# Performance work log

Measured on AMD Instinct MI355X. Metric: run time of the kernel, lower is better.

## Reference

```python
import jax, jax.numpy as jnp
import numpy as np

NEG_SLOPE = 0.01  # torch leaky_relu default
EPS = 1e-12      # torch F.normalize default


def _edge_mlp(edge_attr, w1, b1, w2, b2, d_h):
    # Sequential(Linear, ReLU, Linear) -> per-edge weight matrices [E, d_h, d_h]
    h = jax.nn.relu(edge_attr @ w1 + b1)
    return (h @ w2 + b2).reshape(-1, d_h, d_h)


def _nnconv(h, src, dst, w_edge, root, bias, n_nodes):
    # message_j->i = x_j @ Theta(e_ji); aggregate (add) at dst; add root transform + bias
    msg = jnp.einsum('ei,eio->eo', h[src], w_edge)  # [E, d_h]
    agg = jax.ops.segment_sum(msg, dst, num_segments=n_nodes)
    return agg + h @ root + bias


def setup_inputs() -> dict:
    key = jax.random.key(0)
    ks = jax.random.split(key, 20)
    N, E, G = 20000, 200000, 128
    d_node, d_edge, d_h, d_out = 64, 16, 32, 32

    x = jax.random.normal(ks[0], (N, d_node), dtype=jnp.float32)
    edge_index = jax.random.randint(ks[1], (2, E), 0, N, dtype=jnp.int32)
    edge_attr = jax.random.normal(ks[2], (E, d_edge), dtype=jnp.float32)
    batch = jnp.sort(jax.random.randint(ks[3], (N,), 0, G, dtype=jnp.int32))

    def lin(k, fan_in, fan_out):
        kw, kb = jax.random.split(k)
        s = 1.0 / np.sqrt(fan_in)
        w = jax.random.uniform(kw, (fan_in, fan_out), jnp.float32, -s, s)
        b = jax.random.uniform(kb, (fan_out,), jnp.float32, -s, s)
        return w, b

    nfc_w, nfc_b = lin(ks[4], d_node, d_h)
    efc1_w1, efc1_b1 = lin(ks[5], d_edge, d_h)
    efc1_w2, efc1_b2 = lin(ks[6], d_h, d_h * d_h)
    root1 = jax.random.uniform(ks[7], (d_h, d_h), jnp.float32, -1/np.sqrt(d_h), 1/np.sqrt(d_h))
    bias1 = jnp.zeros((d_h,), jnp.float32)
    efc2_w1, efc2_b1 = lin(ks[8], d_edge, d_h)
    efc2_w2, efc2_b2 = lin(ks[9], d_h, d_h * d_h)
    root2 = jax.random.uniform(ks[10], (d_h, d_h), jnp.float32, -1/np.sqrt(d_h), 1/np.sqrt(d_h))
    bias2 = jnp.zeros((d_h,), jnp.float32)
    fc_w, fc_b = lin(ks[11], d_h, d_out)

    return dict(x=x, edge_index=edge_index, edge_attr=edge_attr, batch=batch,
                num_graphs=G,
                nfc_w=nfc_w, nfc_b=nfc_b,
                efc1_w1=efc1_w1, efc1_b1=efc1_b1, efc1_w2=efc1_w2, efc1_b2=efc1_b2,
                root1=root1, bias1=bias1,
                efc2_w1=efc2_w1, efc2_b1=efc2_b1, efc2_w2=efc2_w2, efc2_b2=efc2_b2,
                root2=root2, bias2=bias2,
                fc_w=fc_w, fc_b=fc_b)


def reference(x, edge_index, edge_attr, batch, num_graphs,
              nfc_w, nfc_b,
              efc1_w1, efc1_b1, efc1_w2, efc1_b2, root1, bias1,
              efc2_w1, efc2_b1, efc2_w2, efc2_b2, root2, bias2,
              fc_w, fc_b):
    n_nodes = x.shape[0]
    d_h = nfc_w.shape[1]
    src, dst = edge_index[0], edge_index[1]

    lrelu = lambda v: jax.nn.leaky_relu(v, NEG_SLOPE)
    # dropout(p=0.1) is identity at inference
    h = lrelu(x @ nfc_w + nfc_b)

    w_e1 = _edge_mlp(edge_attr, efc1_w1, efc1_b1, efc1_w2, efc1_b2, d_h)
    h = lrelu(_nnconv(h, src, dst, w_e1, root1, bias1, n_nodes))

    w_e2 = _edge_mlp(edge_attr, efc2_w1, efc2_b1, efc2_w2, efc2_b2, d_h)
    atom_embs = lrelu(_nnconv(h, src, dst, w_e2, root2, bias2, n_nodes))

    pooled = jax.ops.segment_sum(atom_embs, batch, num_segments=num_graphs)  # [G, d_h]
    norm = jnp.linalg.norm(pooled, ord=2, axis=1, keepdims=True)
    pooled = pooled / jnp.maximum(norm, EPS)

    out = pooled @ fc_w + fc_b
    return (out, atom_embs)
```

## Files before the change

### kernel.cpp

```cpp
#include <hip/hip_runtime.h>
#include <stdint.h>

#define NN 20000
#define NE 200000
#define NG 128
#define NJOBS 6250
#define SLOTS 2048

typedef __attribute__((ext_vector_type(8))) short short8;
typedef __attribute__((ext_vector_type(4))) float f32x4;
typedef __attribute__((ext_vector_type(4))) int   int4v;
typedef __attribute__((ext_vector_type(2))) unsigned int uint2v;

static __device__ __forceinline__ float bf2f(short s) {
    union { unsigned int u; float f; } x;
    x.u = ((unsigned int)(unsigned short)s) << 16;
    return x.f;
}
static __device__ __forceinline__ unsigned short f2bf(float f) {
    unsigned int u = __builtin_bit_cast(unsigned int, f);
    u += 0x7fffu + ((u >> 16) & 1u);
    return (unsigned short)(u >> 16);
}
static __device__ __forceinline__ unsigned int pack2bf(float a, float b) {
    unsigned int u0 = __builtin_bit_cast(unsigned int, a) + 0x8000u;
    unsigned int u1 = __builtin_bit_cast(unsigned int, b) + 0x8000u;
    return __builtin_amdgcn_perm(u1, u0, 0x07060302u);
}
static __device__ __forceinline__ int detect_isbf(const unsigned int* x) {
    unsigned int u = x[threadIdx.x & 63];
    unsigned int el = (u >> 7) & 0xffu;
    unsigned long long bm = __ballot((el >= 100u) && (el <= 140u));
    return __popcll(bm) > 32;
}

__global__ __launch_bounds__(256) void k_prep(
    const void* w2a, const void* b2a, const void* w2b, const void* b2b,
    const void* w1a, const void* b1a, const void* w1b, const void* b1b,
    const void* ea, const unsigned int* xdet,
    short* __restrict__ W2Ta, short* __restrict__ W2Tb,
    short* __restrict__ w1t_ws, float* __restrict__ b1f_ws,
    float* __restrict__ pooled, short* __restrict__ ea_ws) {
    const int isbf = detect_isbf(xdet);
    if (blockIdx.x == 0) {
        for (int i = threadIdx.x; i < NG * 32; i += 256) pooled[i] = 0.f;
    }
    if (blockIdx.x == 1) {
        for (int i = threadIdx.x; i < 1024; i += 256) {
            int layer = i >> 9, jj = i & 511, c = jj >> 4, q = jj & 15;
            const void* w1p = layer ? w1b : w1a;
            w1t_ws[i] = isbf ? ((const short*)w1p)[q * 32 + c]
                             : (short)f2bf(((const float*)w1p)[q * 32 + c]);
        }
        for (int i = threadIdx.x; i < 64; i += 256) {
            int layer = i >> 5, c = i & 31;
            const void* b1p = layer ? b1b : b1a;
            b1f_ws[i] = isbf ? bf2f(((const short*)b1p)[c])
                             : ((const float*)b1p)[c];
        }
    }
    int t = blockIdx.x * 256 + threadIdx.x;
    if (t < 2 * 32 * 1056) {
        int layer = t / (32 * 1056);
        int r = t - layer * (32 * 1056);
        int o = r / 1056, kp = r - o * 1056;
        const void* w2 = layer ? w2b : w2a;
        const void* b2 = layer ? b2b : b2a;
        int idx; const void* sp;
        if (kp < 1024) { int kk = kp >> 5, i = kp & 31; idx = kk * 1024 + i * 32 + o; sp = w2; }
        else           { int i = kp - 1024;             idx = i * 32 + o;             sp = b2; }
        short v = isbf ? ((const short*)sp)[idx] : (short)f2bf(((const float*)sp)[idx]);
        (layer ? W2Tb : W2Ta)[o * 1056 + kp] = v;
        return;
    }
    int u = t - 2 * 32 * 1056;
    if (u < NE * 2 && !isbf) {
        const float* p = (const float*)ea + (size_t)u * 8;
        f32x4 f0 = *(const f32x4*)p;
        f32x4 f1 = *(const f32x4*)(p + 4);
        union { unsigned int d[4]; short8 v; } o8;
        o8.d[0] = pack2bf(f0[0], f0[1]);
        o8.d[1] = pack2bf(f0[2], f0[3]);
        o8.d[2] = pack2bf(f1[0], f1[1]);
        o8.d[3] = pack2bf(f1[2], f1[3]);
        *(short8*)&ea_ws[(size_t)u * 8] = o8.v;
    }
}

__global__ __launch_bounds__(256) void k_node_embed_agg(
    const void* x, const void* w, const void* b,
    const void* root, const void* bias,
    float* __restrict__ h0, float* __restrict__ agg) {
    const int isbf = detect_isbf((const unsigned int*)x);
    __shared__ float wf[64 * 32];
    __shared__ float rf[32 * 32];
    __shared__ float bfs[32];
    __shared__ float rb[32];
    __shared__ float hrow[8][33];
    for (int i = threadIdx.x; i < 64 * 32; i += 256)
        wf[i] = isbf ? bf2f(((const short*)w)[i]) : ((const float*)w)[i];
    for (int i = threadIdx.x; i < 32 * 32; i += 256)
        rf[i] = isbf ? bf2f(((const short*)root)[i]) : ((const float*)root)[i];
    if (threadIdx.x < 32) {
        bfs[threadIdx.x] = isbf ? bf2f(((const short*)b)[threadIdx.x])
                                : ((const float*)b)[threadIdx.x];
        rb[threadIdx.x]  = isbf ? bf2f(((const short*)bias)[threadIdx.x])
                                : ((const float*)bias)[threadIdx.x];
    }
    __syncthreads();
    int t = blockIdx.x * 256 + threadIdx.x;
    if (t >= NN * 32) return;
    int v = t >> 5, c = t & 31, vl = threadIdx.x >> 5;
    float acc = bfs[c];
    if (isbf) {
        const short* xr = (const short*)x + (size_t)v * 64;
#pragma unroll
        for (int q = 0; q < 64; ++q) acc += bf2f(xr[q]) * wf[q * 32 + c];
    } else {
        const float* xr = (const float*)x + (size_t)v * 64;
#pragma unroll
        for (int q = 0; q < 64; ++q) acc += xr[q] * wf[q * 32 + c];
    }
    float hv = acc > 0.f ? acc : 0.01f * acc;
    h0[t] = hv;
    hrow[vl][c] = hv;
    __syncthreads();
    float a2 = rb[c];
#pragma unroll
    for (int q = 0; q < 32; ++q) a2 += hrow[vl][q] * rf[q * 32 + c];
    agg[t] = a2;
}

__global__ __launch_bounds__(256) void k_mid(
    const float* __restrict__ aggA, const void* root, const void* bias,
    const unsigned int* xdet, float* __restrict__ h1b, float* __restrict__ aggB) {
    const int isbf = detect_isbf(xdet);
    __shared__ float rf[32 * 32];
    __shared__ float bfs[32];
    for (int i = threadIdx.x; i < 1024; i += 256)
        rf[i] = isbf ? bf2f(((const short*)root)[i]) : ((const float*)root)[i];
    if (threadIdx.x < 32)
        bfs[threadIdx.x] = isbf ? bf2f(((const short*)bias)[threadIdx.x])
                                : ((const float*)bias)[threadIdx.x];
    __syncthreads();
    int t = blockIdx.x * 256 + threadIdx.x;
    if (t >= NN * 32) return;
    int v = t >> 5, c = t & 31;
    const float* ar = aggA + v * 32;
    float acc = bfs[c];
    float own = 0.f;
#pragma unroll
    for (int q = 0; q < 32; ++q) {
        float hv = ar[q];
        hv = hv > 0.f ? hv : 0.01f * hv;
        if (q == c) own = hv;
        acc += hv * rf[q * 32 + c];
    }
    h1b[t] = own;
    aggB[t] = acc;
}

__global__ __launch_bounds__(256, 4) void k_edge(
    const float* __restrict__ h_in,
    const short* __restrict__ W2T,
    const short* __restrict__ w1pre,
    const float* __restrict__ b1pre,
    const int* __restrict__ src, const int* __restrict__ dst,
    const short* __restrict__ ea_bf,
    const short* __restrict__ ea_ws,
    const unsigned int* xdet,
    float* agg) {
    __shared__ __align__(16) short w2t[32 * 546];
    __shared__ __align__(16) short h1l[4 * 16 * 36];

    const int isbf = detect_isbf(xdet);
    const short* eap = isbf ? ea_bf : ea_ws;

    const int half = blockIdx.x & 1;
    const int k0   = half ? 512 : 0;
    const int S17  = half;
    const int KS   = 546;
    const int KLEN = half ? 544 : 512;

    {
        int cpr = KLEN >> 3;
        int chunks = 32 * cpr;
        for (int idx = threadIdx.x; idx < chunks; idx += 256) {
            int o = idx / cpr, t8 = idx - o * cpr;
            *(short8*)&w2t[o * KS + (t8 << 3)] =
                *(const short8*)&W2T[o * 1056 + k0 + (t8 << 3)];
        }
    }
    __syncthreads();

    const int lane = threadIdx.x & 63;
    const int wid  = threadIdx.x >> 6;
    const int m    = lane & 15;
    const int quad = lane >> 4;
    const int wb   = wid * (16 * 36);

    short8 w1frag = {0, 0, 0, 0, 0, 0, 0, 0};
    if (quad < 2) {
        int c = m + (half << 4);
        w1frag = *(const short8*)&w1pre[c * 16 + ((quad & 1) << 3)];
    }
    const float b1v = b1pre[m + (half << 4)];
    const f32x4 zero4 = {0.f, 0.f, 0.f, 0.f};

    int j = (blockIdx.x >> 1) * 4 + wid;

    short8 eafc[2];
    f32x4 hs[2][2];
    int srcn[2];
    int4v dvc[2];
    {
        const int e0 = j << 5;
        int s0[2];
#pragma unroll
        for (int mt = 0; mt < 2; ++mt) {
            eafc[mt] = *(const short8*)&eap[(size_t)(e0 + mt * 16 + m) * 16 + ((quad & 1) << 3)];
            s0[mt] = src[e0 + mt * 16 + m];
        }
#pragma unroll
        for (int mt = 0; mt < 2; ++mt) {
            const float* hr = h_in + (size_t)s0[mt] * 32 + (quad << 3);
            hs[mt][0] = *(const f32x4*)hr;
            hs[mt][1] = *(const f32x4*)(hr + 4);
        }
#pragma unroll
        for (int mt = 0; mt < 2; ++mt)
            dvc[mt] = *(const int4v*)&dst[e0 + mt * 16 + (quad << 2)];
        const int en = (j + SLOTS) < NJOBS ? ((j + SLOTS) << 5) : 0;
#pragma unroll
        for (int mt = 0; mt < 2; ++mt) srcn[mt] = src[en + mt * 16 + m];
    }

    while (j < NJOBS) {
        const int jn = j + SLOTS;

#pragma unroll
        for (int mt = 0; mt < 2; ++mt) {
            f32x4 hacc = __builtin_amdgcn_mfma_f32_16x16x32_bf16(
                eafc[mt], w1frag, zero4, 0, 0, 0);
            float v0 = fmaxf(hacc[0] + b1v, 0.f);
            float v1 = fmaxf(hacc[1] + b1v, 0.f);
            float v2 = fmaxf(hacc[2] + b1v, 0.f);
            float v3 = fmaxf(hacc[3] + b1v, 0.f);
            uint2v dl; dl[0] = pack2bf(v0, v1); dl[1] = pack2bf(v2, v3);
            *(uint2v*)&h1l[wb + m * 36 + (mt << 4) + (quad << 2)] = dl;
        }
        __asm volatile("s_waitcnt lgkmcnt(0)" ::: "memory");

        if (jn < NJOBS) {
            const int en = jn << 5;
#pragma unroll
            for (int mt = 0; mt < 2; ++mt)
                eafc[mt] = *(const short8*)&eap[(size_t)(en + mt * 16 + m) * 16 + ((quad & 1) << 3)];
        }

        short8 hsbf[2];
#pragma unroll
        for (int mt = 0; mt < 2; ++mt) {
            union { unsigned int du[4]; short8 v; } a;
#pragma unroll
            for (int p = 0; p < 4; ++p) {
                f32x4 hv = hs[mt][p >> 1];
                a.du[p] = pack2bf(hv[(p & 1) * 2], hv[(p & 1) * 2 + 1]);
            }
            hsbf[mt] = a.v;
        }

        int4v dvn[2] = {dvc[0], dvc[1]};
        if (jn < NJOBS) {
#pragma unroll
            for (int mt = 0; mt < 2; ++mt) {
                const float* hr = h_in + (size_t)srcn[mt] * 32 + (quad << 3);
                hs[mt][0] = *(const f32x4*)hr;
                hs[mt][1] = *(const f32x4*)(hr + 4);
            }
            const int en = jn << 5;
#pragma unroll
            for (int mt = 0; mt < 2; ++mt)
                dvn[mt] = *(const int4v*)&dst[en + mt * 16 + (quad << 2)];
            const int jn2 = jn + SLOTS;
            if (jn2 < NJOBS) {
                const int en2 = jn2 << 5;
#pragma unroll
                for (int mt = 0; mt < 2; ++mt) srcn[mt] = src[en2 + mt * 16 + m];
            }
        }

        f32x4 acc0[2], acc1[2];
#pragma unroll
        for (int mt = 0; mt < 2; ++mt) { acc0[mt] = zero4; acc1[mt] = zero4; }

#pragma unroll
        for (int s = 0; s < 16; ++s) {
            short8 bf0 = *(const short8*)&w2t[m * KS + (s << 5) + (quad << 3)];
            short8 bf1 = *(const short8*)&w2t[(m + 16) * KS + (s << 5) + (quad << 3)];
#pragma unroll
            for (int mt = 0; mt < 2; ++mt) {
                uint2v hd = *(const uint2v*)&h1l[wb + s * 36 + (mt << 4) + (quad << 2)];
                f32x4 hv;
                hv[0] = __builtin_bit_cast(float, hd[0] << 16);
                hv[1] = __builtin_bit_cast(float, hd[0] & 0xffff0000u);
                hv[2] = __builtin_bit_cast(float, hd[1] << 16);
                hv[3] = __builtin_bit_cast(float, hd[1] & 0xffff0000u);
                f32x4 u0 = __builtin_amdgcn_mfma_f32_16x16x32_bf16(hsbf[mt], bf0, zero4, 0, 0, 0);
                f32x4 u1 = __builtin_amdgcn_mfma_f32_16x16x32_bf16(hsbf[mt], bf1, zero4, 0, 0, 0);
                acc0[mt] += hv * u0;
                acc1[mt] += hv * u1;
            }
        }
        if (S17) {
            const int s = 16;
            short8 bf0 = *(const short8*)&w2t[m * KS + (s << 5) + (quad << 3)];
            short8 bf1 = *(const short8*)&w2t[(m + 16) * KS + (s << 5) + (quad << 3)];
#pragma unroll
            for (int mt = 0; mt < 2; ++mt) {
                acc0[mt] = __builtin_amdgcn_mfma_f32_16x16x32_bf16(hsbf[mt], bf0, acc0[mt], 0, 0, 0);
                acc1[mt] = __builtin_amdgcn_mfma_f32_16x16x32_bf16(hsbf[mt], bf1, acc1[mt], 0, 0, 0);
            }
        }

#pragma unroll
        for (int mt = 0; mt < 2; ++mt) {
#pragma unroll
            for (int r = 0; r < 4; ++r) {
                float* ap = agg + (size_t)dvc[mt][r] * 32 + m;
                atomicAdd(ap, acc0[mt][r]);
                atomicAdd(ap + 16, acc1[mt][r]);
            }
        }
        dvc[0] = dvn[0];
        dvc[1] = dvn[1];
        j = jn;
    }
}

__global__ __launch_bounds__(256) void k_final_nodes(
    const float* __restrict__ agg, const int* __restrict__ batch,
    const unsigned int* xdet, void* __restrict__ out, float* pooled) {
    const int isbf = detect_isbf(xdet);
    __shared__ float gacc[8][32];
    __shared__ int g0s;
    ((float*)gacc)[threadIdx.x] = 0.f;
    if (threadIdx.x == 0) g0s = batch[blockIdx.x * 8];
    __syncthreads();
    int t = blockIdx.x * 256 + threadIdx.x;
    float v = agg[t];
    v = v > 0.f ? v : 0.01f * v;
    if (isbf) ((short*)out)[4096 + t] = (short)f2bf(v);
    else      ((float*)out)[4096 + t] = v;
    int g = batch[t >> 5];
    int rel = g - g0s;
    int c = t & 31;
    if (rel < 8) atomicAdd(&gacc[rel][c], v);
    else         atomicAdd(&pooled[g * 32 + c], v);
    __syncthreads();
    {
        int gi = threadIdx.x >> 5, cc = threadIdx.x & 31;
        float s = gacc[gi][cc];
        if (s != 0.f) atomicAdd(&pooled[(g0s + gi) * 32 + cc], s);
    }
}

__global__ __launch_bounds__(64) void k_graph_out(
    const float* __restrict__ pooled, const void* fcw, const void* fcb,
    const unsigned int* xdet, void* __restrict__ out) {
    const int isbf = detect_isbf(xdet);
    int g = blockIdx.x;
    int t = threadIdx.x;
    __shared__ float pn[32];
    if (t < 32) {
        float p = pooled[g * 32 + t];
        float sq = p * p;
#pragma unroll
        for (int o = 16; o > 0; o >>= 1) sq += __shfl_xor(sq, o, 64);
        float inv = 1.0f / fmaxf(sqrtf(sq), 1e-12f);
        pn[t] = p * inv;
    }
    __syncthreads();
    if (t < 32) {
        float acc = isbf ? bf2f(((const short*)fcb)[t]) : ((const float*)fcb)[t];
#pragma unroll
        for (int q = 0; q < 32; ++q) {
            float wv = isbf ? bf2f(((const short*)fcw)[q * 32 + t])
                            : ((const float*)fcw)[q * 32 + t];
            acc += pn[q] * wv;
        }
        if (isbf) ((short*)out)[g * 32 + t] = (short)f2bf(acc);
        else      ((float*)out)[g * 32 + t] = acc;
    }
}

extern "C" void kernel_launch(void* const* d_in, const int* in_sizes, int n_in,
                              void* d_out, int out_size, void* d_ws, size_t ws_size,
                              hipStream_t stream) {
    (void)in_sizes; (void)n_in; (void)out_size; (void)ws_size;
    const void* x     = d_in[0];
    const int*  eidx  = (const int*)d_in[1];
    const void* ea    = d_in[2];
    const int*  batch = (const int*)d_in[3];
    const void* nfcw  = d_in[5];
    const void* nfcb  = d_in[6];
    const void* e1w1  = d_in[7];
    const void* e1b1  = d_in[8];
    const void* e1w2  = d_in[9];
    const void* e1b2  = d_in[10];
    const void* root1 = d_in[11];
    const void* bias1 = d_in[12];
    const void* e2w1  = d_in[13];
    const void* e2b1  = d_in[14];
    const void* e2w2  = d_in[15];
    const void* e2b2  = d_in[16];
    const void* root2 = d_in[17];
    const void* bias2 = d_in[18];
    const void* fcw   = d_in[19];
    const void* fcb   = d_in[20];
    const unsigned int* xdet = (const unsigned int*)x;

    char* ws = (char*)d_ws;
    float* h0     = (float*)ws; ws += (size_t)NN * 32 * 4;
    float* h1b    = (float*)ws; ws += (size_t)NN * 32 * 4;
    float* aggA   = (float*)ws; ws += (size_t)NN * 32 * 4;
    float* aggB   = (float*)ws; ws += (size_t)NN * 32 * 4;
    short* W2T1   = (short*)ws; ws += 32 * 1056 * 2;
    short* W2T2   = (short*)ws; ws += 32 * 1056 * 2;
    short* w1t_ws = (short*)ws; ws += 1024 * 2;
    float* b1f_ws = (float*)ws; ws += 64 * 4;
    float* pooled = (float*)ws; ws += NG * 32 * 4;
    short* ea_ws  = (short*)ws; ws += (size_t)NE * 16 * 2;

    const int* srcp = eidx;
    const int* dstp = eidx + NE;

    k_prep<<<(67584 + 400000 + 255) / 256, 256, 0, stream>>>(
        e1w2, e1b2, e2w2, e2b2, e1w1, e1b1, e2w1, e2b1, ea, xdet,
        W2T1, W2T2, w1t_ws, b1f_ws, pooled, ea_ws);
    k_node_embed_agg<<<(NN * 32 + 255) / 256, 256, 0, stream>>>(
        x, nfcw, nfcb, root1, bias1, h0, aggA);

    k_edge<<<1024, 256, 0, stream>>>(h0, W2T1, w1t_ws, b1f_ws, srcp, dstp,
                                     (const short*)ea, ea_ws, xdet, aggA);
    k_mid<<<(NN * 32 + 255) / 256, 256, 0, stream>>>(aggA, root2, bias2, xdet, h1b, aggB);
    k_edge<<<1024, 256, 0, stream>>>(h1b, W2T2, w1t_ws + 512, b1f_ws + 32, srcp, dstp,
                                     (const short*)ea, ea_ws, xdet, aggB);
    k_final_nodes<<<(NN * 32 + 255) / 256, 256, 0, stream>>>(aggB, batch, xdet, d_out, pooled);
    k_graph_out<<<NG, 64, 0, stream>>>(pooled, fcw, fcb, xdet, d_out);
}
```

Baseline: 237.5 us.

## Fuse prep/embed, mid and graph-out kernels; shrink edge jobs to 16 edges

Merges the weight/edge-attr prep and node embedding into one launch, which also zeroes aggB. The layer-2 root transform and leaky-relu move into the second edge kernel: the root term is atomically added to aggB, and leaky-relu is applied to gathered aggA rows, so h1b is no longer needed. The graph-output kernel is folded into the final node kernel via a last-block counter. Edge jobs shrink from 32 to 16 edges each, doubling the job count. This removes three launches and a full node pass. The cost is extra atomics and recomputing leaky-relu on every gathered row, and the smaller jobs reduce per-iteration work, which may hurt latency hiding.

```diff
diff --git a/kernel.cpp b/kernel.cpp
--- a/kernel.cpp
+++ b/kernel.cpp
@@ -4,8 +4,9 @@
 #define NN 20000
 #define NE 200000
 #define NG 128
-#define NJOBS 6250
+#define NJOBS 12500
 #define SLOTS 2048
+#define FINBLKS 2500
 
 typedef __attribute__((ext_vector_type(8))) short short8;
 typedef __attribute__((ext_vector_type(4))) float f32x4;
@@ -34,130 +35,114 @@
     return __popcll(bm) > 32;
 }
 
-__global__ __launch_bounds__(256) void k_prep(
+__global__ __launch_bounds__(256) void k_prep_all(
+    const void* x, const void* nfcw, const void* nfcb,
+    const void* root1, const void* bias1,
     const void* w2a, const void* b2a, const void* w2b, const void* b2b,
     const void* w1a, const void* b1a, const void* w1b, const void* b1b,
-    const void* ea, const unsigned int* xdet,
+    const void* ea,
+    float* __restrict__ h0, float* __restrict__ aggA, float* __restrict__ aggB,
     short* __restrict__ W2Ta, short* __restrict__ W2Tb,
     short* __restrict__ w1t_ws, float* __restrict__ b1f_ws,
-    float* __restrict__ pooled, short* __restrict__ ea_ws) {
-    const int isbf = detect_isbf(xdet);
-    if (blockIdx.x == 0) {
-        for (int i = threadIdx.x; i < NG * 32; i += 256) pooled[i] = 0.f;
-    }
-    if (blockIdx.x == 1) {
-        for (int i = threadIdx.x; i < 1024; i += 256) {
-            int layer = i >> 9, jj = i & 511, c = jj >> 4, q = jj & 15;
-            const void* w1p = layer ? w1b : w1a;
-            w1t_ws[i] = isbf ? ((const short*)w1p)[q * 32 + c]
-                             : (short)f2bf(((const float*)w1p)[q * 32 + c]);
-        }
-        for (int i = threadIdx.x; i < 64; i += 256) {
-            int layer = i >> 5, c = i & 31;
-            const void* b1p = layer ? b1b : b1a;
-            b1f_ws[i] = isbf ? bf2f(((const short*)b1p)[c])
-                             : ((const float*)b1p)[c];
-        }
-    }
-    int t = blockIdx.x * 256 + threadIdx.x;
-    if (t < 2 * 32 * 1056) {
-        int layer = t / (32 * 1056);
-        int r = t - layer * (32 * 1056);
-        int o = r / 1056, kp = r - o * 1056;
-        const void* w2 = layer ? w2b : w2a;
-        const void* b2 = layer ? b2b : b2a;
-        int idx; const void* sp;
-        if (kp < 1024) { int kk = kp >> 5, i = kp & 31; idx = kk * 1024 + i * 32 + o; sp = w2; }
-        else           { int i = kp - 1024;             idx = i * 32 + o;             sp = b2; }
-        short v = isbf ? ((const short*)sp)[idx] : (short)f2bf(((const float*)sp)[idx]);
-        (layer ? W2Tb : W2Ta)[o * 1056 + kp] = v;
+    float* __restrict__ pooled, short* __restrict__ ea_ws,
+    int* __restrict__ finctr) {
+    const int isbf = detect_isbf((const unsigned int*)x);
+    const int b = blockIdx.x;
+
+    if (b < 2500) {
+        __shared__ float wf[64 * 32];
+        __shared__ float rf[32 * 32];
+        __shared__ float bfs[32];
+        __shared__ float rb[32];
+        __shared__ float hrow[8][33];
+        for (int i = threadIdx.x; i < 64 * 32; i += 256)
+            wf[i] = isbf ? bf2f(((const short*)nfcw)[i]) : ((const float*)nfcw)[i];
+        for (int i = threadIdx.x; i < 32 * 32; i += 256)
+            rf[i] = isbf ? bf2f(((const short*)root1)[i]) : ((const float*)root1)[i];
+        if (threadIdx.x < 32) {
+            bfs[threadIdx.x] = isbf ? bf2f(((const short*)nfcb)[threadIdx.x])
+                                    : ((const float*)nfcb)[threadIdx.x];
+            rb[threadIdx.x]  = isbf ? bf2f(((const short*)bias1)[threadIdx.x])
+                                    : ((const float*)bias1)[threadIdx.x];
+        }
+        __syncthreads();
+        int t = b * 256 + threadIdx.x;
+        int v = t >> 5, c = t & 31, vl = threadIdx.x >> 5;
+        float acc = bfs[c];
+        if (isbf) {
+            const short* xr = (const short*)x + (size_t)v * 64;
+#pragma unroll
+            for (int q = 0; q < 64; ++q) acc += bf2f(xr[q]) * wf[q * 32 + c];
+        } else {
+            const float* xr = (const float*)x + (size_t)v * 64;
+#pragma unroll
+            for (int q = 0; q < 64; ++q) acc += xr[q] * wf[q * 32 + c];
+        }
+        float hv = acc > 0.f ? acc : 0.01f * acc;
+        h0[t] = hv;
+        hrow[vl][c] = hv;
+        __syncthreads();
+        float a2 = rb[c];
+#pragma unroll
+        for (int q = 0; q < 32; ++q) a2 += hrow[vl][q] * rf[q * 32 + c];
+        aggA[t] = a2;
         return;
     }
-    int u = t - 2 * 32 * 1056;
-    if (u < NE * 2 && !isbf) {
-        const float* p = (const float*)ea + (size_t)u * 8;
-        f32x4 f0 = *(const f32x4*)p;
-        f32x4 f1 = *(const f32x4*)(p + 4);
-        union { unsigned int d[4]; short8 v; } o8;
-        o8.d[0] = pack2bf(f0[0], f0[1]);
-        o8.d[1] = pack2bf(f0[2], f0[3]);
-        o8.d[2] = pack2bf(f1[0], f1[1]);
-        o8.d[3] = pack2bf(f1[2], f1[3]);
-        *(short8*)&ea_ws[(size_t)u * 8] = o8.v;
-    }
-}
-
-__global__ __launch_bounds__(256) void k_node_embed_agg(
-    const void* x, const void* w, const void* b,
-    const void* root, const void* bias,
-    float* __restrict__ h0, float* __restrict__ agg) {
-    const int isbf = detect_isbf((const unsigned int*)x);
-    __shared__ float wf[64 * 32];
-    __shared__ float rf[32 * 32];
-    __shared__ float bfs[32];
-    __shared__ float rb[32];
-    __shared__ float hrow[8][33];
-    for (int i = threadIdx.x; i < 64 * 32; i += 256)
-        wf[i] = isbf ? bf2f(((const short*)w)[i]) : ((const float*)w)[i];
-    for (int i = threadIdx.x; i < 32 * 32; i += 256)
-        rf[i] = isbf ? bf2f(((const short*)root)[i]) : ((const float*)root)[i];
-    if (threadIdx.x < 32) {
-        bfs[threadIdx.x] = isbf ? bf2f(((const short*)b)[threadIdx.x])
-                                : ((const float*)b)[threadIdx.x];
-        rb[threadIdx.x]  = isbf ? bf2f(((const short*)bias)[threadIdx.x])
-                                : ((const float*)bias)[threadIdx.x];
-    }
-    __syncthreads();
-    int t = blockIdx.x * 256 + threadIdx.x;
-    if (t >= NN * 32) return;
-    int v = t >> 5, c = t & 31, vl = threadIdx.x >> 5;
-    float acc = bfs[c];
-    if (isbf) {
-        const short* xr = (const short*)x + (size_t)v * 64;
-#pragma unroll
-        for (int q = 0; q < 64; ++q) acc += bf2f(xr[q]) * wf[q * 32 + c];
-    } else {
-        const float* xr = (const float*)x + (size_t)v * 64;
-#pragma unroll
-        for (int q = 0; q < 64; ++q) acc += xr[q] * wf[q * 32 + c];
-    }
-    float hv = acc > 0.f ? acc : 0.01f * acc;
-    h0[t] = hv;
-    hrow[vl][c] = hv;
-    __syncthreads();
-    float a2 = rb[c];
-#pragma unroll
-    for (int q = 0; q < 32; ++q) a2 += hrow[vl][q] * rf[q * 32 + c];
-    agg[t] = a2;
-}
-
-__global__ __launch_bounds__(256) void k_mid(
-    const float* __restrict__ aggA, const void* root, const void* bias,
-    const unsigned int* xdet, float* __restrict__ h1b, float* __restrict__ aggB) {
-    const int isbf = detect_isbf(xdet);
-    __shared__ float rf[32 * 32];
-    __shared__ float bfs[32];
-    for (int i = threadIdx.x; i < 1024; i += 256)
-        rf[i] = isbf ? bf2f(((const short*)root)[i]) : ((const float*)root)[i];
-    if (threadIdx.x < 32)
-        bfs[threadIdx.x] = isbf ? bf2f(((const short*)bias)[threadIdx.x])
-                                : ((const float*)bias)[threadIdx.x];
-    __syncthreads();
-    int t = blockIdx.x * 256 + threadIdx.x;
-    if (t >= NN * 32) return;
-    int v = t >> 5, c = t & 31;
-    const float* ar = aggA + v * 32;
-    float acc = bfs[c];
-    float own = 0.f;
-#pragma unroll
-    for (int q = 0; q < 32; ++q) {
-        float hv = ar[q];
-        hv = hv > 0.f ? hv : 0.01f * hv;
-        if (q == c) own = hv;
-        acc += hv * rf[q * 32 + c];
-    }
-    h1b[t] = own;
-    aggB[t] = acc;
+    if (b < 4327) {
+        const int bb = b - 2500;
+        if (bb == 0) {
+            for (int i = threadIdx.x; i < NG * 32; i += 256) pooled[i] = 0.f;
+            if (threadIdx.x == 0) *finctr = 0;
+        }
+        if (bb == 1) {
+            for (int i = threadIdx.x; i < 1024; i += 256) {
+                int layer = i >> 9, jj = i & 511, c = jj >> 4, q = jj & 15;
+                const void* w1p = layer ? w1b : w1a;
+                w1t_ws[i] = isbf ? ((const short*)w1p)[q * 32 + c]
+                                 : (short)f2bf(((const float*)w1p)[q * 32 + c]);
+            }
+            for (int i = threadIdx.x; i < 64; i += 256) {
+                int layer = i >> 5, c = i & 31;
+                const void* b1p = layer ? b1b : b1a;
+                b1f_ws[i] = isbf ? bf2f(((const short*)b1p)[c])
+                                 : ((const float*)b1p)[c];
+            }
+        }
+        int t = bb * 256 + threadIdx.x;
+        if (t < 2 * 32 * 1056) {
+            int layer = t / (32 * 1056);
+            int r = t - layer * (32 * 1056);
+            int o = r / 1056, kp = r - o * 1056;
+            const void* w2 = layer ? w2b : w2a;
+            const void* b2 = layer ? b2b : b2a;
+            int idx; const void* sp;
+            if (kp < 1024) { int kk = kp >> 5, i = kp & 31; idx = kk * 1024 + i * 32 + o; sp = w2; }
+            else           { int i = kp - 1024;             idx = i * 32 + o;             sp = b2; }
+            short v = isbf ? ((const short*)sp)[idx] : (short)f2bf(((const float*)sp)[idx]);
+            (layer ? W2Tb : W2Ta)[o * 1056 + kp] = v;
+            return;
+        }
+        int u = t - 2 * 32 * 1056;
+        if (u < NE * 2 && !isbf) {
+            const float* p = (const float*)ea + (size_t)u * 8;
+            f32x4 f0 = *(const f32x4*)p;
+            f32x4 f1 = *(const f32x4*)(p + 4);
+            union { unsigned int d[4]; short8 v; } o8;
+            o8.d[0] = pack2bf(f0[0], f0[1]);
+            o8.d[1] = pack2bf(f0[2], f0[3]);
+            o8.d[2] = pack2bf(f1[0], f1[1]);
+            o8.d[3] = pack2bf(f1[2], f1[3]);
+            *(short8*)&ea_ws[(size_t)u * 8] = o8.v;
+        }
+        return;
+    }
+    {
+        int idx = (b - 4327) * 256 + threadIdx.x;
+        if (idx < NN * 32 / 4) {
+            f32x4 z = {0.f, 0.f, 0.f, 0.f};
+            ((f32x4*)aggB)[idx] = z;
+        }
+    }
 }
 
 __global__ __launch_bounds__(256, 4) void k_edge(
@@ -169,9 +154,10 @@
     const short* __restrict__ ea_bf,
     const short* __restrict__ ea_ws,
     const unsigned int* xdet,
-    float* agg) {
+    float* agg,
+    const int layer2, const void* rootp, const void* biasp) {
     __shared__ __align__(16) short w2t[32 * 546];
-    __shared__ __align__(16) short h1l[4 * 16 * 36];
+    __shared__ __align__(16) short h1l[4 * 16 * 20];
 
     const int isbf = detect_isbf(xdet);
     const short* eap = isbf ? ea_bf : ea_ws;
@@ -191,13 +177,32 @@
                 *(const short8*)&W2T[o * 1056 + k0 + (t8 << 3)];
         }
     }
+
+    if (layer2) {
+        const int base = blockIdx.x * 625;
+        for (int i = threadIdx.x; i < 625; i += 256) {
+            int t = base + i;
+            int v = t >> 5, c = t & 31;
+            const float* ar = h_in + (size_t)v * 32;
+            float acc = isbf ? bf2f(((const short*)biasp)[c]) : ((const float*)biasp)[c];
+#pragma unroll
+            for (int q = 0; q < 32; ++q) {
+                float hv = ar[q];
+                hv = hv > 0.f ? hv : 0.01f * hv;
+                float wv = isbf ? bf2f(((const short*)rootp)[q * 32 + c])
+                                : ((const float*)rootp)[q * 32 + c];
+                acc += hv * wv;
+            }
+            atomicAdd(&agg[t], acc);
+        }
+    }
     __syncthreads();
 
     const int lane = threadIdx.x & 63;
     const int wid  = threadIdx.x >> 6;
     const int m    = lane & 15;
     const int quad = lane >> 4;
-    const int wb   = wid * (16 * 36);
+    const int wb   = wid * (16 * 20);
 
     short8 w1frag = {0, 0, 0, 0, 0, 0, 0, 0};
     if (quad < 2) {
@@ -209,141 +214,113 @@
 
     int j = (blockIdx.x >> 1) * 4 + wid;
 
-    short8 eafc[2];
-    f32x4 hs[2][2];
-    int srcn[2];
-    int4v dvc[2];
+    short8 eafc;
+    f32x4 hs[2];
+    int srcn;
+    int4v dvc;
     {
-        const int e0 = j << 5;
-        int s0[2];
-#pragma unroll
-        for (int mt = 0; mt < 2; ++mt) {
-            eafc[mt] = *(const short8*)&eap[(size_t)(e0 + mt * 16 + m) * 16 + ((quad & 1) << 3)];
-            s0[mt] = src[e0 + mt * 16 + m];
-        }
-#pragma unroll
-        for (int mt = 0; mt < 2; ++mt) {
-            const float* hr = h_in + (size_t)s0[mt] * 32 + (quad << 3);
-            hs[mt][0] = *(const f32x4*)hr;
-            hs[mt][1] = *(const f32x4*)(hr + 4);
-        }
-#pragma unroll
-        for (int mt = 0; mt < 2; ++mt)
-            dvc[mt] = *(const int4v*)&dst[e0 + mt * 16 + (quad << 2)];
-        const int en = (j + SLOTS) < NJOBS ? ((j + SLOTS) << 5) : 0;
-#pragma unroll
-        for (int mt = 0; mt < 2; ++mt) srcn[mt] = src[en + mt * 16 + m];
+        const int e0 = j << 4;
+        eafc = *(const short8*)&eap[(size_t)(e0 + m) * 16 + ((quad & 1) << 3)];
+        int s0 = src[e0 + m];
+        const float* hr = h_in + (size_t)s0 * 32 + (quad << 3);
+        hs[0] = *(const f32x4*)hr;
+        hs[1] = *(const f32x4*)(hr + 4);
+        dvc = *(const int4v*)&dst[e0 + (quad << 2)];
+        const int en = (j + SLOTS) < NJOBS ? ((j + SLOTS) << 4) : 0;
+        srcn = src[en + m];
     }
 
     while (j < NJOBS) {
         const int jn = j + SLOTS;
 
-#pragma unroll
-        for (int mt = 0; mt < 2; ++mt) {
+        {
             f32x4 hacc = __builtin_amdgcn_mfma_f32_16x16x32_bf16(
-                eafc[mt], w1frag, zero4, 0, 0, 0);
+                eafc, w1frag, zero4, 0, 0, 0);
             float v0 = fmaxf(hacc[0] + b1v, 0.f);
             float v1 = fmaxf(hacc[1] + b1v, 0.f);
             float v2 = fmaxf(hacc[2] + b1v, 0.f);
             float v3 = fmaxf(hacc[3] + b1v, 0.f);
             uint2v dl; dl[0] = pack2bf(v0, v1); dl[1] = pack2bf(v2, v3);
-            *(uint2v*)&h1l[wb + m * 36 + (mt << 4) + (quad << 2)] = dl;
+            *(uint2v*)&h1l[wb + m * 20 + (quad << 2)] = dl;
         }
         __asm volatile("s_waitcnt lgkmcnt(0)" ::: "memory");
 
         if (jn < NJOBS) {
-            const int en = jn << 5;
-#pragma unroll
-            for (int mt = 0; mt < 2; ++mt)
-                eafc[mt] = *(const short8*)&eap[(size_t)(en + mt * 16 + m) * 16 + ((quad & 1) << 3)];
-        }
-
-        short8 hsbf[2];
-#pragma unroll
-        for (int mt = 0; mt < 2; ++mt) {
+            const int en = jn << 4;
+            eafc = *(const short8*)&eap[(size_t)(en + m) * 16 + ((quad & 1) << 3)];
+        }
+
+        short8 hsbf;
+        {
+            f32x4 g0 = hs[0], g1 = hs[1];
+            if (layer2) {
+#pragma unroll
+                for (int p = 0; p < 4; ++p) {
+                    g0[p] = g0[p] > 0.f ? g0[p] : 0.01f * g0[p];
+                    g1[p] = g1[p] > 0.f ? g1[p] : 0.01f * g1[p];
+                }
+            }
             union { unsigned int du[4]; short8 v; } a;
-#pragma unroll
-            for (int p = 0; p < 4; ++p) {
-                f32x4 hv = hs[mt][p >> 1];
-                a.du[p] = pack2bf(hv[(p & 1) * 2], hv[(p & 1) * 2 + 1]);
-            }
-            hsbf[mt] = a.v;
-        }
-
-        int4v dvn[2] = {dvc[0], dvc[1]};
+            a.du[0] = pack2bf(g0[0], g0[1]);
+            a.du[1] = pack2bf(g0[2], g0[3]);
+            a.du[2] = pack2bf(g1[0], g1[1]);
+            a.du[3] = pack2bf(g1[2], g1[3]);
+            hsbf = a.v;
+        }
+
+        int4v dvn = dvc;
         if (jn < NJOBS) {
-#pragma unroll
-            for (int mt = 0; mt < 2; ++mt) {
-                const float* hr = h_in + (size_t)srcn[mt] * 32 + (quad << 3);
-                hs[mt][0] = *(const f32x4*)hr;
-                hs[mt][1] = *(const f32x4*)(hr + 4);
-            }
-            const int en = jn << 5;
-#pragma unroll
-            for (int mt = 0; mt < 2; ++mt)
-                dvn[mt] = *(const int4v*)&dst[en + mt * 16 + (quad << 2)];
+            const float* hr = h_in + (size_t)srcn * 32 + (quad << 3);
+            hs[0] = *(const f32x4*)hr;
+            hs[1] = *(const f32x4*)(hr + 4);
+            dvn = *(const int4v*)&dst[(jn << 4) + (quad << 2)];
             const int jn2 = jn + SLOTS;
-            if (jn2 < NJOBS) {
-                const int en2 = jn2 << 5;
-#pragma unroll
-                for (int mt = 0; mt < 2; ++mt) srcn[mt] = src[en2 + mt * 16 + m];
-            }
-        }
-
-        f32x4 acc0[2], acc1[2];
-#pragma unroll
-        for (int mt = 0; mt < 2; ++mt) { acc0[mt] = zero4; acc1[mt] = zero4; }
-
+            if (jn2 < NJOBS) srcn = src[(jn2 << 4) + m];
+        }
+
+        f32x4 acc0 = zero4, acc1 = zero4;
 #pragma unroll
         for (int s = 0; s < 16; ++s) {
             short8 bf0 = *(const short8*)&w2t[m * KS + (s << 5) + (quad << 3)];
             short8 bf1 = *(const short8*)&w2t[(m + 16) * KS + (s << 5) + (quad << 3)];
-#pragma unroll
-            for (int mt = 0; mt < 2; ++mt) {
-                uint2v hd = *(const uint2v*)&h1l[wb + s * 36 + (mt << 4) + (quad << 2)];
-                f32x4 hv;
-                hv[0] = __builtin_bit_cast(float, hd[0] << 16);
-                hv[1] = __builtin_bit_cast(float, hd[0] & 0xffff0000u);
-                hv[2] = __builtin_bit_cast(float, hd[1] << 16);
-                hv[3] = __builtin_bit_cast(float, hd[1] & 0xffff0000u);
-                f32x4 u0 = __builtin_amdgcn_mfma_f32_16x16x32_bf16(hsbf[mt], bf0, zero4, 0, 0, 0);
-                f32x4 u1 = __builtin_amdgcn_mfma_f32_16x16x32_bf16(hsbf[mt], bf1, zero4, 0, 0, 0);
-                acc0[mt] += hv * u0;
-                acc1[mt] += hv * u1;
-            }
+            uint2v hd = *(const uint2v*)&h1l[wb + s * 20 + (quad << 2)];
+            f32x4 hv;
+            hv[0] = __builtin_bit_cast(float, hd[0] << 16);
+            hv[1] = __builtin_bit_cast(float, hd[0] & 0xffff0000u);
+            hv[2] = __builtin_bit_cast(float, hd[1] << 16);
+            hv[3] = __builtin_bit_cast(float, hd[1] & 0xffff0000u);
+            f32x4 u0 = __builtin_amdgcn_mfma_f32_16x16x32_bf16(hsbf, bf0, zero4, 0, 0, 0);
+            f32x4 u1 = __builtin_amdgcn_mfma_f32_16x16x32_bf16(hsbf, bf1, zero4, 0, 0, 0);
+            acc0 += hv * u0;
+            acc1 += hv * u1;
         }
         if (S17) {
             const int s = 16;
             short8 bf0 = *(const short8*)&w2t[m * KS + (s << 5) + (quad << 3)];
             short8 bf1 = *(const short8*)&w2t[(m + 16) * KS + (s << 5) + (quad << 3)];
-#pragma unroll
-            for (int mt = 0; mt < 2; ++mt) {
-                acc0[mt] = __builtin_amdgcn_mfma_f32_16x16x32_bf16(hsbf[mt], bf0, acc0[mt], 0, 0, 0);
-                acc1[mt] = __builtin_amdgcn_mfma_f32_16x16x32_bf16(hsbf[mt], bf1, acc1[mt], 0, 0, 0);
-            }
-        }
-
-#pragma unroll
-        for (int mt = 0; mt < 2; ++mt) {
-#pragma unroll
-            for (int r = 0; r < 4; ++r) {
-                float* ap = agg + (size_t)dvc[mt][r] * 32 + m;
-                atomicAdd(ap, acc0[mt][r]);
-                atomicAdd(ap + 16, acc1[mt][r]);
-            }
-        }
-        dvc[0] = dvn[0];
-        dvc[1] = dvn[1];
+            acc0 = __builtin_amdgcn_mfma_f32_16x16x32_bf16(hsbf, bf0, acc0, 0, 0, 0);
+            acc1 = __builtin_amdgcn_mfma_f32_16x16x32_bf16(hsbf, bf1, acc1, 0, 0, 0);
+        }
+
+#pragma unroll
+        for (int r = 0; r < 4; ++r) {
+            float* ap = agg + (size_t)dvc[r] * 32 + m;
+            atomicAdd(ap, acc0[r]);
+            atomicAdd(ap + 16, acc1[r]);
+        }
+        dvc = dvn;
         j = jn;
     }
 }
 
-__global__ __launch_bounds__(256) void k_final_nodes(
+__global__ __launch_bounds__(256) void k_final(
     const float* __restrict__ agg, const int* __restrict__ batch,
-    const unsigned int* xdet, void* __restrict__ out, float* pooled) {
+    const unsigned int* xdet, void* __restrict__ out, float* pooled,
+    const void* fcw, const void* fcb, int* __restrict__ finctr) {
     const int isbf = detect_isbf(xdet);
     __shared__ float gacc[8][32];
     __shared__ int g0s;
+    __shared__ int lastf;
     ((float*)gacc)[threadIdx.x] = 0.f;
     if (threadIdx.x == 0) g0s = batch[blockIdx.x * 8];
     __syncthreads();
@@ -363,34 +340,32 @@
         float s = gacc[gi][cc];
         if (s != 0.f) atomicAdd(&pooled[(g0s + gi) * 32 + cc], s);
     }
-}
-
-__global__ __launch_bounds__(64) void k_graph_out(
-    const float* __restrict__ pooled, const void* fcw, const void* fcb,
-    const unsigned int* xdet, void* __restrict__ out) {
-    const int isbf = detect_isbf(xdet);
-    int g = blockIdx.x;
-    int t = threadIdx.x;
-    __shared__ float pn[32];
-    if (t < 32) {
-        float p = pooled[g * 32 + t];
+    __threadfence();
+    __syncthreads();
+    if (threadIdx.x == 0) lastf = (atomicAdd(finctr, 1) == FINBLKS - 1);
+    __syncthreads();
+    if (!lastf) return;
+
+    int lane32 = threadIdx.x & 31;
+    int grp = threadIdx.x >> 5;
+    for (int gb = 0; gb < NG; gb += 8) {
+        int gg = gb + grp;
+        float p = atomicAdd(&pooled[gg * 32 + lane32], 0.0f);
         float sq = p * p;
 #pragma unroll
-        for (int o = 16; o > 0; o >>= 1) sq += __shfl_xor(sq, o, 64);
+        for (int o = 16; o > 0; o >>= 1) sq += __shfl_xor(sq, o, 32);
         float inv = 1.0f / fmaxf(sqrtf(sq), 1e-12f);
-        pn[t] = p * inv;
-    }
-    __syncthreads();
-    if (t < 32) {
-        float acc = isbf ? bf2f(((const short*)fcb)[t]) : ((const float*)fcb)[t];
+        float pn = p * inv;
+        float acc = isbf ? bf2f(((const short*)fcb)[lane32]) : ((const float*)fcb)[lane32];
 #pragma unroll
         for (int q = 0; q < 32; ++q) {
-            float wv = isbf ? bf2f(((const short*)fcw)[q * 32 + t])
-                            : ((const float*)fcw)[q * 32 + t];
-            acc += pn[q] * wv;
-        }
-        if (isbf) ((short*)out)[g * 32 + t] = (short)f2bf(acc);
-        else      ((float*)out)[g * 32 + t] = acc;
+            float pq = __shfl(pn, q, 32);
+            float wv = isbf ? bf2f(((const short*)fcw)[q * 32 + lane32])
+                            : ((const float*)fcw)[q * 32 + lane32];
+            acc += pq * wv;
+        }
+        if (isbf) ((short*)out)[gg * 32 + lane32] = (short)f2bf(acc);
+        else      ((float*)out)[gg * 32 + lane32] = acc;
     }
 }
 
@@ -422,7 +397,6 @@
 
     char* ws = (char*)d_ws;
     float* h0     = (float*)ws; ws += (size_t)NN * 32 * 4;
-    float* h1b    = (float*)ws; ws += (size_t)NN * 32 * 4;
     float* aggA   = (float*)ws; ws += (size_t)NN * 32 * 4;
     float* aggB   = (float*)ws; ws += (size_t)NN * 32 * 4;
     short* W2T1   = (short*)ws; ws += 32 * 1056 * 2;
@@ -431,21 +405,22 @@
     float* b1f_ws = (float*)ws; ws += 64 * 4;
     float* pooled = (float*)ws; ws += NG * 32 * 4;
     short* ea_ws  = (short*)ws; ws += (size_t)NE * 16 * 2;
+    int*   finctr = (int*)ws;   ws += sizeof(int);
 
     const int* srcp = eidx;
     const int* dstp = eidx + NE;
 
-    k_prep<<<(67584 + 400000 + 255) / 256, 256, 0, stream>>>(
-        e1w2, e1b2, e2w2, e2b2, e1w1, e1b1, e2w1, e2b1, ea, xdet,
-        W2T1, W2T2, w1t_ws, b1f_ws, pooled, ea_ws);
-    k_node_embed_agg<<<(NN * 32 + 255) / 256, 256, 0, stream>>>(
-        x, nfcw, nfcb, root1, bias1, h0, aggA);
+    k_prep_all<<<4952, 256, 0, stream>>>(
+        x, nfcw, nfcb, root1, bias1,
+        e1w2, e1b2, e2w2, e2b2, e1w1, e1b1, e2w1, e2b1, ea,
+        h0, aggA, aggB, W2T1, W2T2, w1t_ws, b1f_ws, pooled, ea_ws, finctr);
 
     k_edge<<<1024, 256, 0, stream>>>(h0, W2T1, w1t_ws, b1f_ws, srcp, dstp,
-                                     (const short*)ea, ea_ws, xdet, aggA);
-    k_mid<<<(NN * 32 + 255) / 256, 256, 0, stream>>>(aggA, root2, bias2, xdet, h1b, aggB);
-    k_edge<<<1024, 256, 0, stream>>>(h1b, W2T2, w1t_ws + 512, b1f_ws + 32, srcp, dstp,
-                                     (const short*)ea, ea_ws, xdet, aggB);
-    k_final_nodes<<<(NN * 32 + 255) / 256, 256, 0, stream>>>(aggB, batch, xdet, d_out, pooled);
-    k_graph_out<<<NG, 64, 0, stream>>>(pooled, fcw, fcb, xdet, d_out);
-}
+                                     (const short*)ea, ea_ws, xdet, aggA,
+                                     0, nullptr, nullptr);
+    k_edge<<<1024, 256, 0, stream>>>(aggA, W2T2, w1t_ws + 512, b1f_ws + 32, srcp, dstp,
+                                     (const short*)ea, ea_ws, xdet, aggB,
+                                     1, root2, bias2);
+    k_final<<<FINBLKS, 256, 0, stream>>>(aggB, batch, xdet, d_out, pooled,
+                                         fcw, fcb, finctr);
+}
```

Measured after the change: 405.3 us. 70.7% more time.
